# Optimization experiments

Measured on AMD Instinct MI355X. Metric: run time of the kernel, lower is better.

The kernel has to match this reference:

```python
import jax, jax.numpy as jnp
import numpy as np

B, D_IN, N_EXP, D_EXP, TOP_K = 8192, 1024, 8, 1024, 2


def setup_inputs() -> dict:
    key = jax.random.key(0)
    ks = jax.random.split(key, 6)
    s_in = 1.0 / np.sqrt(D_IN)
    s_exp = 1.0 / np.sqrt(D_EXP)
    return {
        "x": jax.random.normal(ks[0], (B, D_IN), jnp.float32),
        "gate_w": jax.random.normal(ks[1], (D_IN, N_EXP), jnp.float32) * s_in,
        "w1": jax.random.normal(ks[2], (N_EXP, D_IN, D_EXP), jnp.float32) * s_in,
        "b1": jax.random.normal(ks[3], (N_EXP, D_EXP), jnp.float32) * 0.01,
        "w2": jax.random.normal(ks[4], (N_EXP, D_EXP, D_EXP), jnp.float32) * s_exp,
        "b2": jax.random.normal(ks[5], (N_EXP, D_EXP), jnp.float32) * 0.01,
    }


def _moe(x, gate_w, w1, b1, w2, b2):
    # Gating: top-k sparse softmax over expert logits.
    gate_logits = x @ gate_w                          # (B, E)
    top_vals, top_idx = jax.lax.top_k(gate_logits, TOP_K)  # (B, K)
    # softmax over only the top-k logits == softmax of -inf-scattered logits
    top_w = jax.nn.softmax(top_vals, axis=-1)          # (B, K)
    gate_weights = jnp.zeros_like(gate_logits).at[
        jnp.arange(x.shape[0])[:, None], top_idx
    ].set(top_w)                                       # (B, E)
    # Dense all-expert MLP (matches torch.stack over experts).
    h = jax.nn.gelu(jnp.einsum("bd,edf->ebf", x, w1) + b1[:, None, :],
                    approximate=False)                 # (E, B, F)
    expert_outs = jnp.einsum("ebf,efg->ebg", h, w2) + b2[:, None, :]  # (E, B, G)
    output = jnp.einsum("be,ebg->bg", gate_weights, expert_outs)      # (B, G)
    return output, gate_weights


def reference(x, gate_w, w1, b1, w2, b2):
    return _moe(x, gate_w, w1, b1, w2, b2)
```

## Files before the change

### kernel.cpp

```cpp
#include <hip/hip_runtime.h>
#include <math.h>
#include <stdint.h>


#define NTOK   8192
#define DIN    1024
#define NEXP   8
#define DEXP   1024
#define MAXROWS 17408
#define MAXTILES 136

typedef __bf16 bf16x8_t __attribute__((ext_vector_type(8)));
typedef float f32x4 __attribute__((ext_vector_type(4)));

__device__ __forceinline__ unsigned short f2bf(float f) {
  union { float f; unsigned int u; } v; v.f = f;
  unsigned int u = v.u;
  u += 0x7fffu + ((u >> 16) & 1u);
  return (unsigned short)(u >> 16);
}

__device__ __forceinline__ float bf2f(unsigned short s) {
  union { unsigned int u; float f; } v; v.u = ((unsigned int)s) << 16;
  return v.f;
}

__device__ __forceinline__ void async16(const void* g, void* l) {
  __builtin_amdgcn_global_load_lds((const __attribute__((address_space(1))) void*)g,
                                   (__attribute__((address_space(3))) void*)l, 16, 0, 0);
}

__device__ __forceinline__ float gelu_fast(float v) {
  float u = v * (1.5957691216057308f + 0.07135481627f * v * v);
  return v * (1.0f / (1.0f + __expf(-u)));
}

__global__ __launch_bounds__(256) void convx_gate_kernel(const float* __restrict__ x,
                                                         const float* __restrict__ gw,
                                                         unsigned short* __restrict__ xbf,
                                                         float* __restrict__ outGate,
                                                         int* __restrict__ topE,
                                                         float* __restrict__ topW) {
  int tid = threadIdx.x, lane = tid & 63, wv = tid >> 6;
  int t = blockIdx.x * 4 + wv;
  const float4* xr = (const float4*)(x + (size_t)t * 1024);
  ushort4* xo = (ushort4*)(xbf + (size_t)t * 1024);
  double acc[NEXP];
  #pragma unroll
  for (int e = 0; e < NEXP; ++e) acc[e] = 0.0;
  #pragma unroll
  for (int j = 0; j < 4; ++j) {
    int q = lane + 64 * j;
    float4 v = xr[q];
    ushort4 r;
    r.x = f2bf(v.x); r.y = f2bf(v.y); r.z = f2bf(v.z); r.w = f2bf(v.w);
    xo[q] = r;
    float vv[4] = {v.x, v.y, v.z, v.w};
    #pragma unroll
    for (int m = 0; m < 4; ++m) {
      int k = q * 4 + m;
      float4 g0 = *(const float4*)(gw + k * 8);
      float4 g1 = *(const float4*)(gw + k * 8 + 4);
      double xv = (double)vv[m];
      acc[0] += xv * (double)g0.x; acc[1] += xv * (double)g0.y;
      acc[2] += xv * (double)g0.z; acc[3] += xv * (double)g0.w;
      acc[4] += xv * (double)g1.x; acc[5] += xv * (double)g1.y;
      acc[6] += xv * (double)g1.z; acc[7] += xv * (double)g1.w;
    }
  }
  #pragma unroll
  for (int off = 32; off > 0; off >>= 1) {
    #pragma unroll
    for (int e = 0; e < NEXP; ++e) acc[e] += __shfl_xor(acc[e], off);
  }
  if (lane == 0) {
    int e0 = 0; double v0 = acc[0];
    #pragma unroll
    for (int e = 1; e < NEXP; ++e) if (acc[e] > v0) { v0 = acc[e]; e0 = e; }
    int e1 = -1; double v1 = -1e300;
    #pragma unroll
    for (int e = 0; e < NEXP; ++e) if (e != e0 && acc[e] > v1) { v1 = acc[e]; e1 = e; }
    float ex = expf((float)(v1 - v0));
    float inv = 1.0f / (1.0f + ex);
    float w0 = inv, w1 = ex * inv;
    float g8[8];
    #pragma unroll
    for (int e = 0; e < NEXP; ++e) g8[e] = 0.f;
    g8[e0] = w0; g8[e1] = w1;
    float4* gp = (float4*)(outGate + t * 8);
    gp[0] = *(float4*)&g8[0];
    gp[1] = *(float4*)&g8[4];
    topE[t * 2 + 0] = e0; topE[t * 2 + 1] = e1;
    topW[t * 2 + 0] = w0; topW[t * 2 + 1] = w1;
  }
}

__global__ __launch_bounds__(256) void transw_kernel(const float* __restrict__ w1,
                                                     const float* __restrict__ w2,
                                                     unsigned short* __restrict__ w1T,
                                                     unsigned short* __restrict__ w2T) {
  int bz = blockIdx.z;
  const float* src = (bz < 8) ? w1 : w2;
  unsigned short* dst = (bz < 8) ? w1T : w2T;
  int e = bz & 7;
  int kt = blockIdx.y, nt = blockIdx.x;
  __shared__ float tile[64][65];
  int tid = threadIdx.x;
  int c = tid & 63, r4 = tid >> 6;
  const float* s = src + (size_t)e * DIN * DEXP;
  #pragma unroll
  for (int i = 0; i < 16; ++i) {
    int r = i * 4 + r4;
    tile[r][c] = s[(size_t)(kt * 64 + r) * 1024 + nt * 64 + c];
  }
  __syncthreads();
  unsigned short* d = dst + (size_t)e * DIN * DEXP;
  #pragma unroll
  for (int i = 0; i < 16; ++i) {
    int r = i * 4 + r4;
    d[(size_t)(nt * 64 + r) * 1024 + kt * 64 + c] = f2bf(tile[c][r]);
  }
}

__global__ __launch_bounds__(1024) void slot_kernel(const int* __restrict__ topE,
                                                    int* __restrict__ topRow,
                                                    int* __restrict__ rowTok,
                                                    int* __restrict__ tileExpert,
                                                    int* __restrict__ tileRowBase) {
  __shared__ int wtot[16][NEXP];
  __shared__ int wbase[16][NEXP];
  __shared__ int soff[NEXP];
  int tid = threadIdx.x, lane = tid & 63, wv = tid >> 6;
  for (int i = tid; i < MAXROWS; i += 1024) rowTok[i] = -1;
  int a0 = tid * 16;
  unsigned long long pk = 0ull;
  int cnt[NEXP];
  #pragma unroll
  for (int e = 0; e < NEXP; ++e) cnt[e] = 0;
  for (int i = 0; i < 16; ++i) {
    int e = topE[a0 + i];
    pk |= (unsigned long long)e << (i * 4);
    cnt[e]++;
  }
  int excl[NEXP];
  #pragma unroll
  for (int e = 0; e < NEXP; ++e) {
    int v = cnt[e], sum = v;
    #pragma unroll
    for (int d = 1; d < 64; d <<= 1) {
      int u = __shfl_up(sum, d);
      if (lane >= d) sum += u;
    }
    excl[e] = sum - v;
    if (lane == 63) wtot[wv][e] = sum;
  }
  __syncthreads();
  if (tid == 0) {
    int counts[NEXP];
    for (int e = 0; e < NEXP; ++e) {
      int s = 0;
      for (int w = 0; w < 16; ++w) { wbase[w][e] = s; s += wtot[w][e]; }
      counts[e] = s;
    }
    int row = 0, tile = 0;
    for (int e = 0; e < NEXP; ++e) {
      soff[e] = row;
      int nt = (counts[e] + 127) >> 7;
      for (int i = 0; i < nt; ++i) { tileExpert[tile] = e; tileRowBase[tile] = row + i * 128; ++tile; }
      row += nt << 7;
    }
    for (; tile < MAXTILES; ++tile) tileExpert[tile] = -1;
  }
  __syncthreads();
  int base[NEXP], run[NEXP];
  #pragma unroll
  for (int e = 0; e < NEXP; ++e) { base[e] = soff[e] + wbase[wv][e] + excl[e]; run[e] = 0; }
  for (int i = 0; i < 16; ++i) {
    int e = (int)((pk >> (i * 4)) & 7ull);
    int row = base[e] + run[e]++;
    rowTok[row] = (a0 + i) >> 1;
    topRow[a0 + i] = row;
  }
}

__global__ __launch_bounds__(256) void gemm1_kernel(const unsigned short* __restrict__ xbf,
                                                    const unsigned short* __restrict__ w1T,
                                                    const float* __restrict__ b1,
                                                    const int* __restrict__ tileExpert,
                                                    const int* __restrict__ tileRowBase,
                                                    const int* __restrict__ rowTok,
                                                    unsigned short* __restrict__ h) {
  int tileId = blockIdx.y;
  int e = tileExpert[tileId];
  if (e < 0) return;
  int rowBase = tileRowBase[tileId];
  int n0 = blockIdx.x * 128;
  __shared__ __align__(16) unsigned short sm[128 * 64 * 2];
  unsigned short* sA = sm;
  unsigned short* sB = sm + 128 * 64;
  int tid = threadIdx.x, lane = tid & 63, wv = tid >> 6;
  int srow = tid >> 3;
  int scolSw = (((tid & 7) ^ ((tid >> 3) & 7)) * 8);
  int tok[4];
  #pragma unroll
  for (int i = 0; i < 4; ++i) {
    int tk = rowTok[rowBase + srow + i * 32];
    tok[i] = tk < 0 ? 0 : tk;
  }
  const unsigned short* Bmat = w1T + (size_t)e * DIN * DEXP;
  int wm = ((tid >> 6) & 1) * 64, wn = (tid >> 7) * 64;
  int rsel = lane & 15, q = lane >> 4;
  int rk = rsel & 7;
  f32x4 acc[4][4] = {};
  for (int kk = 0; kk < DIN; kk += 64) {
    #pragma unroll
    for (int i = 0; i < 4; ++i) {
      int abase = __builtin_amdgcn_readfirstlane((wv * 8 + i * 32) * 128);
      async16(xbf + (size_t)tok[i] * 1024 + kk + scolSw, (char*)sm + abase);
      async16(Bmat + (size_t)(n0 + srow + i * 32) * 1024 + kk + scolSw,
              (char*)sm + abase + 16384);
    }
    __syncthreads();
    #pragma unroll
    for (int ks = 0; ks < 64; ks += 32) {
      int co = (((ks >> 3) + q) ^ rk) * 8;
      bf16x8_t af[4], bfr[4];
      #pragma unroll
      for (int mi = 0; mi < 4; ++mi)
        af[mi] = *(const bf16x8_t*)&sA[(wm + mi * 16 + rsel) * 64 + co];
      #pragma unroll
      for (int ni = 0; ni < 4; ++ni)
        bfr[ni] = *(const bf16x8_t*)&sB[(wn + ni * 16 + rsel) * 64 + co];
      #pragma unroll
      for (int mi = 0; mi < 4; ++mi)
        #pragma unroll
        for (int ni = 0; ni < 4; ++ni)
          acc[mi][ni] = __builtin_amdgcn_mfma_f32_16x16x32_bf16(af[mi], bfr[ni], acc[mi][ni], 0, 0, 0);
    }
    __syncthreads();
  }
  float b1v[4];
  int quad = lane >> 4;
  #pragma unroll
  for (int ni = 0; ni < 4; ++ni) b1v[ni] = b1[e * 1024 + n0 + wn + ni * 16 + rsel];
  #pragma unroll
  for (int mi = 0; mi < 4; ++mi)
    #pragma unroll
    for (int ni = 0; ni < 4; ++ni)
      #pragma unroll
      for (int r = 0; r < 4; ++r) {
        int m = wm + mi * 16 + quad * 4 + r;
        int n = wn + ni * 16 + rsel;
        sm[m * 128 + n] = f2bf(gelu_fast(acc[mi][ni][r] + b1v[ni]));
      }
  __syncthreads();
  #pragma unroll
  for (int i = 0; i < 8; ++i) {
    int idx = i * 2048 + tid * 8;
    int m = idx >> 7, c = idx & 127;
    int g = rowBase + m;
    *(uint4*)(h + (size_t)g * 1024 + n0 + c) = *(const uint4*)&sm[idx];
  }
}

__global__ __launch_bounds__(256) void gemm2_kernel(const unsigned short* __restrict__ h,
                                                    const unsigned short* __restrict__ w2T,
                                                    const float* __restrict__ b2,
                                                    const int* __restrict__ tileExpert,
                                                    const int* __restrict__ tileRowBase,
                                                    unsigned short* __restrict__ y) {
  int tileId = blockIdx.y;
  int e = tileExpert[tileId];
  if (e < 0) return;
  int rowBase = tileRowBase[tileId];
  int n0 = blockIdx.x * 128;
  __shared__ __align__(16) unsigned short sm[128 * 64 * 2];
  unsigned short* sA = sm;
  unsigned short* sB = sm + 128 * 64;
  int tid = threadIdx.x, lane = tid & 63, wv = tid >> 6;
  int srow = tid >> 3;
  int scolSw = (((tid & 7) ^ ((tid >> 3) & 7)) * 8);
  const unsigned short* Bmat = w2T + (size_t)e * DEXP * DEXP;
  int wm = ((tid >> 6) & 1) * 64, wn = (tid >> 7) * 64;
  int rsel = lane & 15, q = lane >> 4;
  int rk = rsel & 7;
  f32x4 acc[4][4] = {};
  for (int kk = 0; kk < DEXP; kk += 64) {
    #pragma unroll
    for (int i = 0; i < 4; ++i) {
      int abase = __builtin_amdgcn_readfirstlane((wv * 8 + i * 32) * 128);
      async16(h + (size_t)(rowBase + srow + i * 32) * 1024 + kk + scolSw, (char*)sm + abase);
      async16(Bmat + (size_t)(n0 + srow + i * 32) * 1024 + kk + scolSw,
              (char*)sm + abase + 16384);
    }
    __syncthreads();
    #pragma unroll
    for (int ks = 0; ks < 64; ks += 32) {
      int co = (((ks >> 3) + q) ^ rk) * 8;
      bf16x8_t af[4], bfr[4];
      #pragma unroll
      for (int mi = 0; mi < 4; ++mi)
        af[mi] = *(const bf16x8_t*)&sA[(wm + mi * 16 + rsel) * 64 + co];
      #pragma unroll
      for (int ni = 0; ni < 4; ++ni)
        bfr[ni] = *(const bf16x8_t*)&sB[(wn + ni * 16 + rsel) * 64 + co];
      #pragma unroll
      for (int mi = 0; mi < 4; ++mi)
        #pragma unroll
        for (int ni = 0; ni < 4; ++ni)
          acc[mi][ni] = __builtin_amdgcn_mfma_f32_16x16x32_bf16(af[mi], bfr[ni], acc[mi][ni], 0, 0, 0);
    }
    __syncthreads();
  }
  float b2v[4];
  int quad = lane >> 4;
  #pragma unroll
  for (int ni = 0; ni < 4; ++ni) b2v[ni] = b2[e * 1024 + n0 + wn + ni * 16 + rsel];
  #pragma unroll
  for (int mi = 0; mi < 4; ++mi)
    #pragma unroll
    for (int ni = 0; ni < 4; ++ni)
      #pragma unroll
      for (int r = 0; r < 4; ++r) {
        int m = wm + mi * 16 + quad * 4 + r;
        int n = wn + ni * 16 + rsel;
        sm[m * 128 + n] = f2bf(acc[mi][ni][r] + b2v[ni]);
      }
  __syncthreads();
  #pragma unroll
  for (int i = 0; i < 8; ++i) {
    int idx = i * 2048 + tid * 8;
    int m = idx >> 7, c = idx & 127;
    int g = rowBase + m;
    *(uint4*)(y + (size_t)g * 1024 + n0 + c) = *(const uint4*)&sm[idx];
  }
}

__global__ __launch_bounds__(256) void combine_kernel(const unsigned short* __restrict__ y,
                                                      const int* __restrict__ topRow,
                                                      const float* __restrict__ topW,
                                                      float* __restrict__ out) {
  int tid = threadIdx.x;
  int wv = tid >> 6, lane = tid & 63;
  int t = blockIdx.x * 4 + wv;
  int r0 = topRow[t * 2 + 0], r1 = topRow[t * 2 + 1];
  float w0 = topW[t * 2 + 0], w1 = topW[t * 2 + 1];
  const unsigned short* p0 = y + (size_t)r0 * 1024 + lane * 16;
  const unsigned short* p1 = y + (size_t)r1 * 1024 + lane * 16;
  float* op = out + (size_t)t * 1024 + lane * 16;
  #pragma unroll
  for (int hh = 0; hh < 2; ++hh) {
    union { uint4 v; unsigned short s[8]; } a, b;
    a.v = *(const uint4*)(p0 + hh * 8);
    b.v = *(const uint4*)(p1 + hh * 8);
    float o[8];
    #pragma unroll
    for (int j = 0; j < 8; ++j)
      o[j] = w0 * bf2f(a.s[j]) + w1 * bf2f(b.s[j]);
    *(float4*)(op + hh * 8) = *(float4*)&o[0];
    *(float4*)(op + hh * 8 + 4) = *(float4*)&o[4];
  }
}

extern "C" void kernel_launch(void* const* d_in, const int* in_sizes, int n_in,
                              void* d_out, int out_size, void* d_ws, size_t ws_size,
                              hipStream_t stream) {
  const float* x  = (const float*)d_in[0];
  const float* gw = (const float*)d_in[1];
  const float* w1 = (const float*)d_in[2];
  const float* b1 = (const float*)d_in[3];
  const float* w2 = (const float*)d_in[4];
  const float* b2 = (const float*)d_in[5];
  float* out = (float*)d_out;

  char* ws = (char*)d_ws;
  int* tileExpert  = (int*)ws;
  int* tileRowBase = tileExpert + MAXTILES;
  int* topE        = tileRowBase + MAXTILES;
  int* topRow      = topE + 16384;
  int* rowTok      = topRow + 16384;
  float* topW      = (float*)(rowTok + MAXROWS);
  unsigned short* xbf  = (unsigned short*)(ws + (512 << 10));
  unsigned short* w1T  = xbf + (size_t)NTOK * DIN;
  unsigned short* w2T  = w1T + (size_t)NEXP * DIN * DEXP;
  unsigned short* hbuf = w2T + (size_t)NEXP * DEXP * DEXP;
  unsigned short* ybuf = hbuf + (size_t)MAXROWS * DEXP;

  transw_kernel<<<dim3(16, 16, 16), 256, 0, stream>>>(w1, w2, w1T, w2T);
  convx_gate_kernel<<<NTOK / 4, 256, 0, stream>>>(x, gw, xbf,
                                                  out + (size_t)NTOK * DEXP, topE, topW);
  slot_kernel<<<1, 1024, 0, stream>>>(topE, topRow, rowTok, tileExpert, tileRowBase);
  gemm1_kernel<<<dim3(8, MAXTILES), 256, 0, stream>>>(xbf, w1T, b1, tileExpert, tileRowBase,
                                                      rowTok, hbuf);
  gemm2_kernel<<<dim3(8, MAXTILES), 256, 0, stream>>>(hbuf, w2T, b2, tileExpert, tileRowBase,
                                                      ybuf);
  combine_kernel<<<NTOK / 4, 256, 0, stream>>>(ybuf, topRow, topW, out);
}
```

Before: 340.2 us.

## Fuse weight transpose, gating and rowTok init into one prep kernel; swap GEMM grid axes

Merges the weight transpose/bf16 kernel, the x conversion plus gating kernel, and the rowTok -1 initialisation into a single prep kernel whose block ranges pick the role. This removes one launch and moves rowTok initialisation out of the single-block slot kernel. The transpose now uses float4 loads and ushort4 stores with a padded tile. The GEMM grids are swapped so consecutive blocks walk row tiles rather than N-chunks, which changes L2 reuse of the expert weights and the order in which blocks are dispatched.

```diff
diff --git a/kernel.cpp b/kernel.cpp
--- a/kernel.cpp
+++ b/kernel.cpp
@@ -35,90 +35,102 @@
   return v * (1.0f / (1.0f + __expf(-u)));
 }
 
-__global__ __launch_bounds__(256) void convx_gate_kernel(const float* __restrict__ x,
-                                                         const float* __restrict__ gw,
-                                                         unsigned short* __restrict__ xbf,
-                                                         float* __restrict__ outGate,
-                                                         int* __restrict__ topE,
-                                                         float* __restrict__ topW) {
-  int tid = threadIdx.x, lane = tid & 63, wv = tid >> 6;
-  int t = blockIdx.x * 4 + wv;
-  const float4* xr = (const float4*)(x + (size_t)t * 1024);
-  ushort4* xo = (ushort4*)(xbf + (size_t)t * 1024);
-  double acc[NEXP];
-  #pragma unroll
-  for (int e = 0; e < NEXP; ++e) acc[e] = 0.0;
-  #pragma unroll
-  for (int j = 0; j < 4; ++j) {
-    int q = lane + 64 * j;
-    float4 v = xr[q];
-    ushort4 r;
-    r.x = f2bf(v.x); r.y = f2bf(v.y); r.z = f2bf(v.z); r.w = f2bf(v.w);
-    xo[q] = r;
-    float vv[4] = {v.x, v.y, v.z, v.w};
-    #pragma unroll
-    for (int m = 0; m < 4; ++m) {
-      int k = q * 4 + m;
-      float4 g0 = *(const float4*)(gw + k * 8);
-      float4 g1 = *(const float4*)(gw + k * 8 + 4);
-      double xv = (double)vv[m];
-      acc[0] += xv * (double)g0.x; acc[1] += xv * (double)g0.y;
-      acc[2] += xv * (double)g0.z; acc[3] += xv * (double)g0.w;
-      acc[4] += xv * (double)g1.x; acc[5] += xv * (double)g1.y;
-      acc[6] += xv * (double)g1.z; acc[7] += xv * (double)g1.w;
-    }
-  }
-  #pragma unroll
-  for (int off = 32; off > 0; off >>= 1) {
-    #pragma unroll
-    for (int e = 0; e < NEXP; ++e) acc[e] += __shfl_xor(acc[e], off);
-  }
-  if (lane == 0) {
-    int e0 = 0; double v0 = acc[0];
-    #pragma unroll
-    for (int e = 1; e < NEXP; ++e) if (acc[e] > v0) { v0 = acc[e]; e0 = e; }
-    int e1 = -1; double v1 = -1e300;
-    #pragma unroll
-    for (int e = 0; e < NEXP; ++e) if (e != e0 && acc[e] > v1) { v1 = acc[e]; e1 = e; }
-    float ex = expf((float)(v1 - v0));
-    float inv = 1.0f / (1.0f + ex);
-    float w0 = inv, w1 = ex * inv;
-    float g8[8];
-    #pragma unroll
-    for (int e = 0; e < NEXP; ++e) g8[e] = 0.f;
-    g8[e0] = w0; g8[e1] = w1;
-    float4* gp = (float4*)(outGate + t * 8);
-    gp[0] = *(float4*)&g8[0];
-    gp[1] = *(float4*)&g8[4];
-    topE[t * 2 + 0] = e0; topE[t * 2 + 1] = e1;
-    topW[t * 2 + 0] = w0; topW[t * 2 + 1] = w1;
-  }
-}
-
-__global__ __launch_bounds__(256) void transw_kernel(const float* __restrict__ w1,
-                                                     const float* __restrict__ w2,
-                                                     unsigned short* __restrict__ w1T,
-                                                     unsigned short* __restrict__ w2T) {
-  int bz = blockIdx.z;
-  const float* src = (bz < 8) ? w1 : w2;
-  unsigned short* dst = (bz < 8) ? w1T : w2T;
-  int e = bz & 7;
-  int kt = blockIdx.y, nt = blockIdx.x;
-  __shared__ float tile[64][65];
+__global__ __launch_bounds__(256) void prep_kernel(const float* __restrict__ x,
+                                                   const float* __restrict__ gw,
+                                                   const float* __restrict__ w1,
+                                                   const float* __restrict__ w2,
+                                                   unsigned short* __restrict__ xbf,
+                                                   unsigned short* __restrict__ w1T,
+                                                   unsigned short* __restrict__ w2T,
+                                                   float* __restrict__ outGate,
+                                                   int* __restrict__ topE,
+                                                   float* __restrict__ topW,
+                                                   int* __restrict__ rowTok) {
+  __shared__ float tile[64][68];
+  int b = blockIdx.x;
   int tid = threadIdx.x;
-  int c = tid & 63, r4 = tid >> 6;
-  const float* s = src + (size_t)e * DIN * DEXP;
-  #pragma unroll
-  for (int i = 0; i < 16; ++i) {
-    int r = i * 4 + r4;
-    tile[r][c] = s[(size_t)(kt * 64 + r) * 1024 + nt * 64 + c];
-  }
-  __syncthreads();
-  unsigned short* d = dst + (size_t)e * DIN * DEXP;
-  #pragma unroll
-  for (int i = 0; i < 16; ++i) {
-    int r = i * 4 + r4;
-    d[(size_t)(nt * 64 + r) * 1024 + kt * 64 + c] = f2bf(tile[c][r]);
+  if (b < 4096) {
+    int z = b >> 8;
+    const float* src = (z < 8) ? w1 : w2;
+    unsigned short* dst = (z < 8) ? w1T : w2T;
+    int e = z & 7;
+    int idx = b & 255, kt = idx >> 4, nt = idx & 15;
+    const float* s = src + (size_t)e * DIN * DEXP + (size_t)kt * 64 * 1024 + nt * 64;
+    unsigned short* d = dst + (size_t)e * DIN * DEXP + (size_t)nt * 64 * 1024 + kt * 64;
+    int c4 = (tid & 15) * 4, r0 = tid >> 4;
+    #pragma unroll
+    for (int p = 0; p < 4; ++p) {
+      int r = r0 + p * 16;
+      *(float4*)&tile[r][c4] = *(const float4*)(s + (size_t)r * 1024 + c4);
+    }
+    __syncthreads();
+    #pragma unroll
+    for (int p = 0; p < 4; ++p) {
+      int nr = r0 + p * 16;
+      ushort4 o;
+      o.x = f2bf(tile[c4 + 0][nr]);
+      o.y = f2bf(tile[c4 + 1][nr]);
+      o.z = f2bf(tile[c4 + 2][nr]);
+      o.w = f2bf(tile[c4 + 3][nr]);
+      *(ushort4*)(d + (size_t)nr * 1024 + c4) = o;
+    }
+  } else if (b < 6144) {
+    int lane = tid & 63, wv = tid >> 6;
+    int t = (b - 4096) * 4 + wv;
+    const float4* xr = (const float4*)(x + (size_t)t * 1024);
+    ushort4* xo = (ushort4*)(xbf + (size_t)t * 1024);
+    double acc[NEXP];
+    #pragma unroll
+    for (int e = 0; e < NEXP; ++e) acc[e] = 0.0;
+    #pragma unroll
+    for (int j = 0; j < 4; ++j) {
+      int q = lane + 64 * j;
+      float4 v = xr[q];
+      ushort4 r;
+      r.x = f2bf(v.x); r.y = f2bf(v.y); r.z = f2bf(v.z); r.w = f2bf(v.w);
+      xo[q] = r;
+      float vv[4] = {v.x, v.y, v.z, v.w};
+      #pragma unroll
+      for (int m = 0; m < 4; ++m) {
+        int k = q * 4 + m;
+        float4 g0 = *(const float4*)(gw + k * 8);
+        float4 g1 = *(const float4*)(gw + k * 8 + 4);
+        double xv = (double)vv[m];
+        acc[0] += xv * (double)g0.x; acc[1] += xv * (double)g0.y;
+        acc[2] += xv * (double)g0.z; acc[3] += xv * (double)g0.w;
+        acc[4] += xv * (double)g1.x; acc[5] += xv * (double)g1.y;
+        acc[6] += xv * (double)g1.z; acc[7] += xv * (double)g1.w;
+      }
+    }
+    #pragma unroll
+    for (int off = 32; off > 0; off >>= 1) {
+      #pragma unroll
+      for (int e = 0; e < NEXP; ++e) acc[e] += __shfl_xor(acc[e], off);
+    }
+    if (lane == 0) {
+      int e0 = 0; double v0 = acc[0];
+      #pragma unroll
+      for (int e = 1; e < NEXP; ++e) if (acc[e] > v0) { v0 = acc[e]; e0 = e; }
+      int e1 = -1; double v1 = -1e300;
+      #pragma unroll
+      for (int e = 0; e < NEXP; ++e) if (e != e0 && acc[e] > v1) { v1 = acc[e]; e1 = e; }
+      float ex = expf((float)(v1 - v0));
+      float inv = 1.0f / (1.0f + ex);
+      float w0 = inv, w1v = ex * inv;
+      float g8[8];
+      #pragma unroll
+      for (int e = 0; e < NEXP; ++e) g8[e] = 0.f;
+      g8[e0] = w0; g8[e1] = w1v;
+      float4* gp = (float4*)(outGate + t * 8);
+      gp[0] = *(float4*)&g8[0];
+      gp[1] = *(float4*)&g8[4];
+      topE[t * 2 + 0] = e0; topE[t * 2 + 1] = e1;
+      topW[t * 2 + 0] = w0; topW[t * 2 + 1] = w1v;
+    }
+  } else {
+    int base = (b - 6144) * 1024 + tid * 4;
+    int4 m1 = make_int4(-1, -1, -1, -1);
+    *(int4*)(rowTok + base) = m1;
   }
 }
 
@@ -131,7 +143,6 @@
   __shared__ int wbase[16][NEXP];
   __shared__ int soff[NEXP];
   int tid = threadIdx.x, lane = tid & 63, wv = tid >> 6;
-  for (int i = tid; i < MAXROWS; i += 1024) rowTok[i] = -1;
   int a0 = tid * 16;
   unsigned long long pk = 0ull;
   int cnt[NEXP];
@@ -190,11 +201,11 @@
                                                     const int* __restrict__ tileRowBase,
                                                     const int* __restrict__ rowTok,
                                                     unsigned short* __restrict__ h) {
-  int tileId = blockIdx.y;
+  int tileId = blockIdx.x;
   int e = tileExpert[tileId];
   if (e < 0) return;
   int rowBase = tileRowBase[tileId];
-  int n0 = blockIdx.x * 128;
+  int n0 = blockIdx.y * 128;
   __shared__ __align__(16) unsigned short sm[128 * 64 * 2];
   unsigned short* sA = sm;
   unsigned short* sB = sm + 128 * 64;
@@ -269,11 +280,11 @@
                                                     const int* __restrict__ tileExpert,
                                                     const int* __restrict__ tileRowBase,
                                                     unsigned short* __restrict__ y) {
-  int tileId = blockIdx.y;
+  int tileId = blockIdx.x;
   int e = tileExpert[tileId];
   if (e < 0) return;
   int rowBase = tileRowBase[tileId];
-  int n0 = blockIdx.x * 128;
+  int n0 = blockIdx.y * 128;
   __shared__ __align__(16) unsigned short sm[128 * 64 * 2];
   unsigned short* sA = sm;
   unsigned short* sB = sm + 128 * 64;
@@ -378,21 +389,21 @@
   int* tileRowBase = tileExpert + MAXTILES;
   int* topE        = tileRowBase + MAXTILES;
   int* topRow      = topE + 16384;
-  int* rowTok      = topRow + 16384;
-  float* topW      = (float*)(rowTok + MAXROWS);
+  float* topW      = (float*)(topRow + 16384);
+  int* rowTok      = (int*)(ws + (256 << 10));
   unsigned short* xbf  = (unsigned short*)(ws + (512 << 10));
   unsigned short* w1T  = xbf + (size_t)NTOK * DIN;
   unsigned short* w2T  = w1T + (size_t)NEXP * DIN * DEXP;
   unsigned short* hbuf = w2T + (size_t)NEXP * DEXP * DEXP;
   unsigned short* ybuf = hbuf + (size_t)MAXROWS * DEXP;
 
-  transw_kernel<<<dim3(16, 16, 16), 256, 0, stream>>>(w1, w2, w1T, w2T);
-  convx_gate_kernel<<<NTOK / 4, 256, 0, stream>>>(x, gw, xbf,
-                                                  out + (size_t)NTOK * DEXP, topE, topW);
+  prep_kernel<<<4096 + 2048 + 17, 256, 0, stream>>>(x, gw, w1, w2, xbf, w1T, w2T,
+                                                    out + (size_t)NTOK * DEXP,
+                                                    topE, topW, rowTok);
   slot_kernel<<<1, 1024, 0, stream>>>(topE, topRow, rowTok, tileExpert, tileRowBase);
-  gemm1_kernel<<<dim3(8, MAXTILES), 256, 0, stream>>>(xbf, w1T, b1, tileExpert, tileRowBase,
+  gemm1_kernel<<<dim3(MAXTILES, 8), 256, 0, stream>>>(xbf, w1T, b1, tileExpert, tileRowBase,
                                                       rowTok, hbuf);
-  gemm2_kernel<<<dim3(8, MAXTILES), 256, 0, stream>>>(hbuf, w2T, b2, tileExpert, tileRowBase,
+  gemm2_kernel<<<dim3(MAXTILES, 8), 256, 0, stream>>>(hbuf, w2T, b2, tileExpert, tileRowBase,
                                                       ybuf);
   combine_kernel<<<NTOK / 4, 256, 0, stream>>>(ybuf, topRow, topW, out);
 }
```

New measurement: 330.4 us. 1.03x faster.
